# Kernel optimization log

Hardware: AMD Instinct MI355X
Metric: run time of the kernel (lower is better)

Reference implementation:

```python
import jax, jax.numpy as jnp
import numpy as np

NEG_SLOPE = 0.2  # LeakyReLU slope used by GAT attention
EPS = 1e-16


def segment_softmax(scores, seg, num_segments):
    # numerically-stable softmax over edges grouped by destination node
    m = jax.ops.segment_max(scores, seg, num_segments=num_segments)
    ex = jnp.exp(scores - m[seg])
    s = jax.ops.segment_sum(ex, seg, num_segments=num_segments)
    return ex / (s[seg] + EPS)


def gat_conv(x, edge_index, W, a_src, a_dst, b):
    # x: [N, d_in], edge_index: [2, E], W: [d_in, d_out], a_*: [d_out], b: [d_out]
    n = x.shape[0]
    h = x @ W                                   # [N, d_out]
    src, dst = edge_index[0], edge_index[1]     # [E], [E]
    alpha_src = h @ a_src                       # [N]
    alpha_dst = h @ a_dst                       # [N]
    e = jax.nn.leaky_relu(alpha_src[src] + alpha_dst[dst], NEG_SLOPE)  # [E]
    alpha = segment_softmax(e, dst, n)          # [E]
    out = jax.ops.segment_sum(h[src] * alpha[:, None], dst, num_segments=n)  # [N, d_out]
    return out + b


def setup_inputs() -> dict:
    key = jax.random.key(0)
    ks = jax.random.split(key, 12)
    N, D, E = 100000, 64, 1600000
    x = jax.random.normal(ks[0], (N, D), dtype=jnp.float32)
    edge_index = jax.random.randint(ks[1], (2, E), 0, N, dtype=jnp.int64)
    s = 1.0 / np.sqrt(D)
    W1 = jax.random.normal(ks[2], (D, D), dtype=jnp.float32) * s
    a_src1 = jax.random.normal(ks[3], (D,), dtype=jnp.float32) * s
    a_dst1 = jax.random.normal(ks[4], (D,), dtype=jnp.float32) * s
    b1 = jnp.zeros((D,), dtype=jnp.float32)
    W2 = jax.random.normal(ks[5], (D, D), dtype=jnp.float32) * s
    a_src2 = jax.random.normal(ks[6], (D,), dtype=jnp.float32) * s
    a_dst2 = jax.random.normal(ks[7], (D,), dtype=jnp.float32) * s
    b2 = jnp.zeros((D,), dtype=jnp.float32)
    return {"x": x, "edge_index": edge_index,
            "W1": W1, "a_src1": a_src1, "a_dst1": a_dst1, "b1": b1,
            "W2": W2, "a_src2": a_src2, "a_dst2": a_dst2, "b2": b2}


def reference(x, edge_index, W1, a_src1, a_dst1, b1, W2, a_src2, a_dst2, b2):
    # Encoder.forward: conv_near on first 500 edges, conv_include on the rest
    x = gat_conv(x, edge_index[:, :500], W1, a_src1, a_dst1, b1)
    return gat_conv(x, edge_index[:, 500:], W2, a_src2, a_dst2, b2)
```

## Files before the change

### kernel.cpp

```cpp
#include <hip/hip_runtime.h>


#define LRELU(v) ((v) >= 0.0f ? (v) : 0.2f * (v))
#define EPSF 1e-16f
#define NB 128
#define BCAP 512

struct P {
    const float* x; const int* EI; int E, N;
    const float *W1, *a_src1, *a_dst1, *b1, *W2, *a_src2, *a_dst2, *b2;
    float* F;
    int* bcnt;
    int* idx_map;
    int* map2;
    float* s_spec;
    float* adsp;
    char* stat;
    float* as2tab; float* ad2tab; float* h2tab;
    int* slw; int* nxt;
    float4* out;
};

__device__ __forceinline__ float wred_sum(float v) {
    for (int o = 32; o; o >>= 1) v += __shfl_xor(v, o);
    return v;
}
__device__ __forceinline__ int wred_min(int v) {
    for (int o = 32; o; o >>= 1) v = min(v, __shfl_xor(v, o));
    return v;
}

__global__ __launch_bounds__(256) void initk(P p) {
    int i = blockIdx.x * 256 + threadIdx.x;
    if (i < p.N) { p.idx_map[i] = -1; p.map2[i] = -1; p.s_spec[i] = 0.f; p.stat[i] = 0; }
    if (i < NB * 16) p.bcnt[i] = 0;
    if (blockIdx.x == 0 && threadIdx.x < 64) {
        int t = threadIdx.x;
        float hb = 0.f;
        for (int k = 0; k < 64; ++k) hb += p.b1[k] * p.W2[k * 64 + t];
        p.F[128 + t] = hb;
        float as = wred_sum(hb * p.a_src2[t]);
        float ad = wred_sum(hb * p.a_dst2[t]);
        if (t == 0) { p.F[192] = as; p.F[193] = ad; }
    }
}

__global__ __launch_bounds__(256) void l1k(P p) {
    const int w = (blockIdx.x * 256 + threadIdx.x) >> 6;
    const int lane = threadIdx.x & 63;
    if (w >= 500) return;

    float wsl = 0.f, wdl = 0.f, hbl = 0.f;
    for (int l = 0; l < 64; ++l) {
        wsl += p.W1[lane * 64 + l] * p.a_src1[l];
        wdl += p.W1[lane * 64 + l] * p.a_dst1[l];
    }
    for (int k = 0; k < 64; ++k) hbl += p.b1[k] * p.W2[k * 64 + lane];

    const int d = p.EI[p.E + w];
    int firstj = 1 << 30;
    for (int r = 0; r < 8; ++r) {
        int j = r * 64 + lane;
        if (j < 500 && p.EI[p.E + j] == d) firstj = min(firstj, j);
    }
    firstj = wred_min(firstj);
    if (firstj != w) return;
    if (lane == 0) p.idx_map[d] = w;

    const float dv = wred_sum(p.x[(long)d * 64 + lane] * wdl);
    float Ssum = 0.f, e1w = 0.f, x1l = 0.f;
    bool fm = true;
    for (int r = 0; r < 8; ++r) {
        int j = r * 64 + lane;
        bool m = (j < 500) && (p.EI[p.E + j] == d);
        unsigned long long mask = __ballot(m);
        while (mask) {
            int j0 = r * 64 + (int)__ffsll(mask) - 1;
            mask &= mask - 1;
            int sj = p.EI[j0];
            float xs = p.x[(long)sj * 64 + lane];
            float e1j = LRELU(wred_sum(xs * wsl) + dv);
            float ew;
            if (fm) { e1w = e1j; ew = 1.f; fm = false; }
            else ew = expf(e1j - e1w);
            Ssum += ew;
            float h1l = 0.f;
            #pragma unroll
            for (int k = 0; k < 64; ++k) h1l = fmaf(__shfl(xs, k), p.W1[k * 64 + lane], h1l);
            x1l = fmaf(ew, h1l, x1l);
        }
    }
    float x1 = x1l / (Ssum + EPSF) + p.b1[lane];
    float h2l = 0.f;
    #pragma unroll
    for (int k = 0; k < 64; ++k) h2l = fmaf(__shfl(x1, k), p.W2[k * 64 + lane], h2l);
    p.h2tab[w * 64 + lane] = h2l - hbl;
    float as = wred_sum(h2l * p.a_src2[lane]);
    float ad = wred_sum(h2l * p.a_dst2[lane]);
    if (lane == 0) { p.as2tab[w] = as; p.ad2tab[w] = ad; }
}

__device__ __forceinline__ void specEdge(const P& p, long e, int s, int bkt,
                                         float asb, float adb) {
    int sl = p.idx_map[s];
    if (sl < 0) return;
    int d = p.EI[p.E + e];
    int jd = p.idx_map[d];
    float ad2v = (jd >= 0) ? p.ad2tab[jd] : adb;
    float md  = LRELU(asb + ad2v);
    float esp = LRELU(p.as2tab[sl] + ad2v);
    atomicAdd(&p.s_spec[d], expf(esp - md) - 1.0f);
    p.stat[d] = 2;
    p.adsp[d] = ad2v;
    int i = atomicAdd(&p.bcnt[bkt * 16], 1);
    if (i < BCAP) {
        int pos = bkt * BCAP + i;
        p.slw[pos] = sl;
        p.nxt[pos] = atomicExch(&p.map2[d], pos);
    }
}

__global__ __launch_bounds__(256) void scanAk(P p) {
    long q = (long)blockIdx.x * 256 + threadIdx.x;
    long base = 500 + q * 4;
    if (base >= p.E) return;
    const float asb = p.F[192], adb = p.F[193];
    int bkt = (int)(q & (NB - 1));
    if (base + 3 < p.E) {
        int4 s4 = *(const int4*)(p.EI + base);
        specEdge(p, base + 0, s4.x, bkt, asb, adb);
        specEdge(p, base + 1, s4.y, bkt, asb, adb);
        specEdge(p, base + 2, s4.z, bkt, asb, adb);
        specEdge(p, base + 3, s4.w, bkt, asb, adb);
    } else {
        for (long e = base; e < p.E; ++e) specEdge(p, e, p.EI[e], bkt, asb, adb);
    }
}

__device__ __forceinline__ void dstEdge(const P& p, int d) {
    char st = p.stat[d];
    if (st == 0) p.stat[d] = 1;
    else if (st == 2) atomicAdd(&p.s_spec[d], 1.0f);
}

__global__ __launch_bounds__(256) void scanBk(P p) {
    long q = (long)blockIdx.x * 256 + threadIdx.x;
    long base = 500 + q * 4;
    if (base >= p.E) return;
    if (base + 3 < p.E) {
        int4 d4 = *(const int4*)(p.EI + p.E + base);
        dstEdge(p, d4.x); dstEdge(p, d4.y); dstEdge(p, d4.z); dstEdge(p, d4.w);
    } else {
        for (long e = base; e < p.E; ++e) dstEdge(p, p.EI[p.E + e]);
    }
}

__global__ __launch_bounds__(256) void outk(P p) {
    long t = (long)blockIdx.x * 256 + threadIdx.x;
    if (t >= (long)p.N * 16) return;
    int n = (int)(t >> 4), qq = (int)(t & 15);
    char st = p.stat[n];
    float coef = (st != 0) ? 1.0f : 0.0f;
    float4 hb4 = ((const float4*)(p.F + 128))[qq];
    float4 b24 = ((const float4*)p.b2)[qq];
    float4 o;
    o.x = b24.x + coef * hb4.x; o.y = b24.y + coef * hb4.y;
    o.z = b24.z + coef * hb4.z; o.w = b24.w + coef * hb4.w;
    if (st == 2) {
        float den = p.s_spec[n] + EPSF;
        float ad2v = p.adsp[n];
        float md = LRELU(p.F[192] + ad2v);
        int pos = p.map2[n];
        while (pos >= 0) {
            int sl = p.slw[pos];
            float w = expf(LRELU(p.as2tab[sl] + ad2v) - md) / den;
            float4 h4 = ((const float4*)(p.h2tab + sl * 64))[qq];
            o.x = fmaf(w, h4.x, o.x); o.y = fmaf(w, h4.y, o.y);
            o.z = fmaf(w, h4.z, o.z); o.w = fmaf(w, h4.w, o.w);
            pos = p.nxt[pos];
        }
    }
    p.out[t] = o;
}

extern "C" void kernel_launch(void* const* d_in, const int* in_sizes, int n_in,
                              void* d_out, int out_size, void* d_ws, size_t ws_size,
                              hipStream_t stream) {
    P p;
    p.x      = (const float*)d_in[0];
    p.EI     = (const int*)d_in[1];
    p.W1     = (const float*)d_in[2];
    p.a_src1 = (const float*)d_in[3];
    p.a_dst1 = (const float*)d_in[4];
    p.b1     = (const float*)d_in[5];
    p.W2     = (const float*)d_in[6];
    p.a_src2 = (const float*)d_in[7];
    p.a_dst2 = (const float*)d_in[8];
    p.b2     = (const float*)d_in[9];
    p.out    = (float4*)d_out;
    p.N = in_sizes[0] / 64;
    p.E = in_sizes[1] / 2;

    char* base = (char*)d_ws;
    p.F       = (float*)base;
    p.bcnt    = (int*)(base + 1024);
    p.idx_map = p.bcnt + NB * 16;
    p.map2    = p.idx_map + p.N;
    p.s_spec  = (float*)(p.map2 + p.N);
    p.adsp    = p.s_spec + p.N;
    p.stat    = (char*)(p.adsp + p.N);
    char* q   = p.stat + p.N;
    q = (char*)(((uintptr_t)q + 63) & ~(uintptr_t)63);
    p.as2tab  = (float*)q;
    p.ad2tab  = p.as2tab + 512;
    p.h2tab   = p.ad2tab + 512;
    p.slw     = (int*)(p.h2tab + 512 * 64);
    p.nxt     = p.slw + NB * BCAP;

    long quads = ((long)p.E - 500 + 3) / 4;
    int scanBlocks = (int)((quads + 255) / 256);

    initk <<<(p.N + 255) / 256, 256, 0, stream>>>(p);
    l1k   <<<125, 256, 0, stream>>>(p);
    scanAk<<<scanBlocks, 256, 0, stream>>>(p);
    scanBk<<<scanBlocks, 256, 0, stream>>>(p);
    outk  <<<(int)(((long)p.N * 16 + 255) / 256), 256, 0, stream>>>(p);
}
```

Measured before the change: 61.57 us.

## Replace per-node idx_map and stat lookups with compact membership bitmaps

Adds 100K-bit source and destination bitmaps (12.5 KB each) that mark the nodes that appear as layer-1 destinations and as destinations of special edges. The 1.6M-edge scans test these cache-resident bitmaps first, so they avoid random reads of the 400 KB idx_map and the char stat array. idx_map is no longer set to -1 at init because it is only read behind a bitmap test. Also vectorizes the W1·a products in l1k with float4 loads and reuses the precomputed b1·W2 vector. The cost is atomicOr traffic on the bitmaps and an unconditional byte write per destination edge.

```diff
diff --git a/kernel.cpp b/kernel.cpp
--- a/kernel.cpp
+++ b/kernel.cpp
@@ -5,6 +5,7 @@
 #define EPSF 1e-16f
 #define NB 128
 #define BCAP 512
+#define BMW 3200
 
 struct P {
     const float* x; const int* EI; int E, N;
@@ -15,7 +16,9 @@
     int* map2;
     float* s_spec;
     float* adsp;
-    char* stat;
+    char* flag;
+    unsigned* srcbm;
+    unsigned* dstbm;
     float* as2tab; float* ad2tab; float* h2tab;
     int* slw; int* nxt;
     float4* out;
@@ -29,10 +32,14 @@
     for (int o = 32; o; o >>= 1) v = min(v, __shfl_xor(v, o));
     return v;
 }
+__device__ __forceinline__ bool bittest(const unsigned* bm, int n) {
+    return (bm[n >> 5] >> (n & 31)) & 1u;
+}
 
 __global__ __launch_bounds__(256) void initk(P p) {
     int i = blockIdx.x * 256 + threadIdx.x;
-    if (i < p.N) { p.idx_map[i] = -1; p.map2[i] = -1; p.s_spec[i] = 0.f; p.stat[i] = 0; }
+    if (i < p.N) { p.map2[i] = -1; p.s_spec[i] = 0.f; p.flag[i] = 0; }
+    if (i < BMW) { p.srcbm[i] = 0u; p.dstbm[i] = 0u; }
     if (i < NB * 16) p.bcnt[i] = 0;
     if (blockIdx.x == 0 && threadIdx.x < 64) {
         int t = threadIdx.x;
@@ -50,12 +57,17 @@
     const int lane = threadIdx.x & 63;
     if (w >= 500) return;
 
-    float wsl = 0.f, wdl = 0.f, hbl = 0.f;
-    for (int l = 0; l < 64; ++l) {
-        wsl += p.W1[lane * 64 + l] * p.a_src1[l];
-        wdl += p.W1[lane * 64 + l] * p.a_dst1[l];
-    }
-    for (int k = 0; k < 64; ++k) hbl += p.b1[k] * p.W2[k * 64 + lane];
+    const float4* W1r = (const float4*)(p.W1 + lane * 64);
+    const float4* as1 = (const float4*)p.a_src1;
+    const float4* ad1 = (const float4*)p.a_dst1;
+    float wsl = 0.f, wdl = 0.f;
+    #pragma unroll
+    for (int l = 0; l < 16; ++l) {
+        float4 wv = W1r[l], av = as1[l], bv = ad1[l];
+        wsl += wv.x * av.x + wv.y * av.y + wv.z * av.z + wv.w * av.w;
+        wdl += wv.x * bv.x + wv.y * bv.y + wv.z * bv.z + wv.w * bv.w;
+    }
+    const float hbl = p.F[128 + lane];
 
     const int d = p.EI[p.E + w];
     int firstj = 1 << 30;
@@ -65,7 +77,10 @@
     }
     firstj = wred_min(firstj);
     if (firstj != w) return;
-    if (lane == 0) p.idx_map[d] = w;
+    if (lane == 0) {
+        p.idx_map[d] = w;
+        atomicOr(&p.srcbm[d >> 5], 1u << (d & 31));
+    }
 
     const float dv = wred_sum(p.x[(long)d * 64 + lane] * wdl);
     float Ssum = 0.f, e1w = 0.f, x1l = 0.f;
@@ -102,16 +117,15 @@
 
 __device__ __forceinline__ void specEdge(const P& p, long e, int s, int bkt,
                                          float asb, float adb) {
+    if (!bittest(p.srcbm, s)) return;
     int sl = p.idx_map[s];
-    if (sl < 0) return;
     int d = p.EI[p.E + e];
-    int jd = p.idx_map[d];
-    float ad2v = (jd >= 0) ? p.ad2tab[jd] : adb;
+    float ad2v = bittest(p.srcbm, d) ? p.ad2tab[p.idx_map[d]] : adb;
     float md  = LRELU(asb + ad2v);
     float esp = LRELU(p.as2tab[sl] + ad2v);
     atomicAdd(&p.s_spec[d], expf(esp - md) - 1.0f);
-    p.stat[d] = 2;
     p.adsp[d] = ad2v;
+    atomicOr(&p.dstbm[d >> 5], 1u << (d & 31));
     int i = atomicAdd(&p.bcnt[bkt * 16], 1);
     if (i < BCAP) {
         int pos = bkt * BCAP + i;
@@ -138,9 +152,8 @@
 }
 
 __device__ __forceinline__ void dstEdge(const P& p, int d) {
-    char st = p.stat[d];
-    if (st == 0) p.stat[d] = 1;
-    else if (st == 2) atomicAdd(&p.s_spec[d], 1.0f);
+    p.flag[d] = 1;
+    if (bittest(p.dstbm, d)) atomicAdd(&p.s_spec[d], 1.0f);
 }
 
 __global__ __launch_bounds__(256) void scanBk(P p) {
@@ -159,14 +172,13 @@
     long t = (long)blockIdx.x * 256 + threadIdx.x;
     if (t >= (long)p.N * 16) return;
     int n = (int)(t >> 4), qq = (int)(t & 15);
-    char st = p.stat[n];
-    float coef = (st != 0) ? 1.0f : 0.0f;
+    float coef = p.flag[n] ? 1.0f : 0.0f;
     float4 hb4 = ((const float4*)(p.F + 128))[qq];
     float4 b24 = ((const float4*)p.b2)[qq];
     float4 o;
     o.x = b24.x + coef * hb4.x; o.y = b24.y + coef * hb4.y;
     o.z = b24.z + coef * hb4.z; o.w = b24.w + coef * hb4.w;
-    if (st == 2) {
+    if (bittest(p.dstbm, n)) {
         float den = p.s_spec[n] + EPSF;
         float ad2v = p.adsp[n];
         float md = LRELU(p.F[192] + ad2v);
@@ -208,10 +220,12 @@
     p.map2    = p.idx_map + p.N;
     p.s_spec  = (float*)(p.map2 + p.N);
     p.adsp    = p.s_spec + p.N;
-    p.stat    = (char*)(p.adsp + p.N);
-    char* q   = p.stat + p.N;
+    p.flag    = (char*)(p.adsp + p.N);
+    char* q   = p.flag + p.N;
     q = (char*)(((uintptr_t)q + 63) & ~(uintptr_t)63);
-    p.as2tab  = (float*)q;
+    p.srcbm   = (unsigned*)q;
+    p.dstbm   = p.srcbm + BMW;
+    p.as2tab  = (float*)(p.dstbm + BMW);
     p.ad2tab  = p.as2tab + 512;
     p.h2tab   = p.ad2tab + 512;
     p.slw     = (int*)(p.h2tab + 512 * 64);
```

New measurement: 59.21 us. 3.8% less time.
